# Optimization experiments

Hardware: AMD Instinct MI355X
Metric: run time of the kernel (lower is better)

## Reference

```python
import jax, jax.numpy as jnp
import numpy as np

HEADDIM = 128
CHUNK = 256


def _ssd_scan(x, dt, A, B, C, chunk):
    # x: (b,l,h,p)  dt: (b,l,h)  A: (h,)  B,C: (b,l,n)  (single group g=1 shared by all heads)
    b, l, h, p = x.shape
    n = B.shape[-1]
    nc = l // chunk
    dA = dt * A  # (b,l,h)
    xc = x.reshape(b, nc, chunk, h, p)
    dtc = dt.reshape(b, nc, chunk, h)
    dAc = dA.reshape(b, nc, chunk, h)
    Bc = B.reshape(b, nc, chunk, n)
    Cc = C.reshape(b, nc, chunk, n)
    cs = jnp.cumsum(dAc, axis=2)  # (b,nc,c,h) cumulative log-decay within chunk
    # intra-chunk quadratic part
    CB = jnp.einsum('bjin,bjkn->bjik', Cc, Bc)  # (b,nc,c,c)
    decay = jnp.exp(cs[:, :, :, None, :] - cs[:, :, None, :, :])  # (b,nc,i,k,h)
    mask = jnp.tril(jnp.ones((chunk, chunk), dtype=bool))
    decay = jnp.where(mask[None, None, :, :, None], decay, 0.0)
    y_intra = jnp.einsum('bjik,bjikh,bjkh,bjkhp->bjihp', CB, decay, dtc, xc)
    # per-chunk end states
    decay_states = jnp.exp(cs[:, :, -1:, :] - cs)  # (b,nc,c,h)
    states = jnp.einsum('bjkh,bjkh,bjkn,bjkhp->bjhnp', decay_states, dtc, Bc, xc)
    # recurrence across chunks: h_j = exp(sum dA_j) * h_{j-1} + states_j
    chunk_decay = jnp.exp(cs[:, :, -1, :])  # (b,nc,h)
    def step(carry, inp):
        s, d = inp
        new = carry * d[:, :, None, None] + s
        return new, carry  # emit state BEFORE this chunk
    init = jnp.zeros((b, h, n, p), x.dtype)
    _, prev = jax.lax.scan(step, init,
                           (states.transpose(1, 0, 2, 3, 4), chunk_decay.transpose(1, 0, 2)))
    prev = prev.transpose(1, 0, 2, 3, 4)  # (b,nc,h,n,p)
    y_inter = jnp.einsum('bjih,bjin,bjhnp->bjihp', jnp.exp(cs), Cc, prev)
    return (y_intra + y_inter).reshape(b, l, h, p)


def setup_inputs() -> dict:
    key = jax.random.key(0)
    k1, k2, k3, k4 = jax.random.split(key, 4)
    b, l, d_inner, nheads, d_state = 2, 4096, 2048, 16, 256
    x = jax.random.normal(k1, (b, l, d_inner), dtype=jnp.float32)
    BC = jax.random.normal(k2, (b, l, 2 * d_state), dtype=jnp.float32) * 0.1
    dt = jax.random.normal(k3, (b, l, 2 * nheads), dtype=jnp.float32) - 3.0
    A_log = jnp.zeros((nheads,), dtype=jnp.float32)
    D = jnp.ones((nheads,), dtype=jnp.float32)
    W_fcD = jax.random.normal(k4, (nheads, d_inner), dtype=jnp.float32) * 0.02
    return {"x": x, "BC": BC, "dt": dt, "A_log": A_log, "D": D, "W_fcD": W_fcD}


def reference(x, BC, dt, A_log, D, W_fcD):
    b, l, dim = x.shape
    h = A_log.shape[0]
    p = HEADDIM
    d_state = BC.shape[-1] // 2
    A = -jnp.exp(A_log)
    # bidirectional: concat forward stream with time-flipped backward stream along batch
    dt2 = jnp.concatenate((dt[:, :, :h], jnp.flip(dt[:, :, h:], axis=1)), axis=0)
    dt2 = jax.nn.softplus(dt2)
    x_og = x
    x2 = jnp.concatenate((x, jnp.flip(x, axis=1)), axis=0)
    BC2 = jnp.concatenate((BC, jnp.flip(BC, axis=1)), axis=0)
    B, C = BC2[..., :d_state], BC2[..., d_state:]
    y = _ssd_scan(x2.reshape(2 * b, l, h, p), dt2, A, B, C, CHUNK)
    y = y.reshape(2 * b, l, dim)
    y = jnp.roll(y, shift=1, axis=1).at[:, 0, :].set(0.0)
    y_fw, y_bw = y[:b], jnp.flip(y[b:], axis=1)
    gate = x_og @ W_fcD.T + D  # (b,l,h)
    y = y_fw + y_bw + x_og * jnp.repeat(gate, p, axis=-1)
    return y
```

## Files before the change

### kernel.cpp

```cpp
#include <hip/hip_runtime.h>
#include <stdint.h>

#define NB 2
#define SL 4096
#define NH 16
#define HD 128
#define DS 256
#define CK 256
#define NCH 16
#define NSQ 4
#define DI 2048

#define EPST 132

typedef unsigned short u16;
typedef unsigned int u32;
typedef __attribute__((ext_vector_type(8))) __bf16 bf16x8;
typedef __attribute__((ext_vector_type(4))) float f32x4;

__device__ __forceinline__ int tor(int dir, int t) { return dir ? (SL - 1 - t) : t; }

__device__ __forceinline__ u16 f2bf(float f) {
  u32 u = __float_as_uint(f);
  u = u + 0x7fffu + ((u >> 16) & 1u);
  return (u16)(u >> 16);
}
__device__ __forceinline__ float bf2f(u16 s) {
  return __uint_as_float(((u32)s) << 16);
}

struct Stg { uint4 a, b; };

__device__ __forceinline__ Stg ld_tile(const u16* __restrict__ src, int row, int q0, int k0) {
  const uint4* p = (const uint4*)(src + (size_t)row * 256 + k0 + (q0 << 3));
  Stg s; s.a = p[0]; s.b = p[1]; return s;
}
__device__ __forceinline__ void st_tile(u16* buf, int row, int q0, Stg s) {
  int sw = (row >> 1) & 3;
  *(uint4*)&buf[row * 32 + ((q0 ^ sw) << 3)] = s.a;
  *(uint4*)&buf[row * 32 + (((q0 + 1) ^ sw) << 3)] = s.b;
}

__device__ __forceinline__ bf16x8 frag(const u16* lds, int base_row, int m, int quad) {
  int row = base_row + m;
  return *(const bf16x8*)&lds[row * 32 + ((quad ^ ((row >> 1) & 3)) << 3)];
}

__device__ __forceinline__ void mfma16(const u16* As, const u16* Bs, int wi, int wp,
                                       int m, int quad, f32x4 acc[4][4]) {
  bf16x8 af[4], bv[4];
#pragma unroll
  for (int r = 0; r < 4; ++r) af[r] = frag(As, wi + (r << 4), m, quad);
#pragma unroll
  for (int c = 0; c < 4; ++c) bv[c] = frag(Bs, wp + (c << 4), m, quad);
#pragma unroll
  for (int r = 0; r < 4; ++r)
#pragma unroll
    for (int c = 0; c < 4; ++c)
      acc[r][c] = __builtin_amdgcn_mfma_f32_16x16x32_bf16(af[r], bv[c], acc[r][c], 0, 0, 0);
}

__global__ __launch_bounds__(256) void kprep(const float* __restrict__ dt,
                                             const float* __restrict__ A_log,
                                             float* __restrict__ csb,
                                             float* __restrict__ dtvb,
                                             float* __restrict__ cdecb) {
  int blk = blockIdx.x;
  int h = blk & 15, sj = blk >> 4;
  int s = sj >> 4, j = sj & 15;
  int b = s & 1, dir = s >> 1;
  int i = threadIdx.x;
  int to = tor(dir, j * CK + i);
  __shared__ float sbuf[CK];
  float a = -expf(A_log[h]);
  float raw = dt[((size_t)(b * SL + to)) * (2 * NH) + dir * NH + h];
  float sp = (raw > 20.f) ? raw : log1pf(expf(raw));
  sbuf[i] = sp * a;
  __syncthreads();
  for (int off = 1; off < CK; off <<= 1) {
    float v = (i >= off) ? sbuf[i - off] : 0.f;
    __syncthreads();
    sbuf[i] += v;
    __syncthreads();
  }
  float csv = sbuf[i];
  size_t base = ((size_t)sj * NH + h) * CK;
  csb[base + i] = csv;
  dtvb[base + i] = sp;
  if (i == CK - 1) cdecb[sj * NH + h] = expf(csv);
}

__global__ __launch_bounds__(256) void kcastT(const float* __restrict__ BC,
                                              u16* __restrict__ Bbf,
                                              u16* __restrict__ Cbf,
                                              u16* __restrict__ BbfT) {
  int blk = blockIdx.x;
  int kq = blk & 3, sj = blk >> 2;
  int s = sj >> 4, j = sj & 15;
  int b = s & 1, dir = s >> 1;
  __shared__ u16 T[64 * 264];
  int tid = threadIdx.x;
  int r = tid >> 2, part = (tid & 3) * 64;
  int t = j * CK + kq * 64 + r;
  int tsrc = tor(dir, t);
  const float* src = BC + ((size_t)(b * SL + tsrc)) * (2 * DS);
  size_t dstb = ((size_t)s * SL + t) * DS;
  u16 bb[64], cc[64];
#pragma unroll
  for (int q = 0; q < 16; ++q) {
    float4 v = ((const float4*)(src + part))[q];
    bb[q * 4 + 0] = f2bf(v.x); bb[q * 4 + 1] = f2bf(v.y);
    bb[q * 4 + 2] = f2bf(v.z); bb[q * 4 + 3] = f2bf(v.w);
    float4 c = ((const float4*)(src + DS + part))[q];
    cc[q * 4 + 0] = f2bf(c.x); cc[q * 4 + 1] = f2bf(c.y);
    cc[q * 4 + 2] = f2bf(c.z); cc[q * 4 + 3] = f2bf(c.w);
  }
#pragma unroll
  for (int q = 0; q < 8; ++q) {
    ((uint4*)(Bbf + dstb + part))[q] = *(const uint4*)&bb[q * 8];
    ((uint4*)(Cbf + dstb + part))[q] = *(const uint4*)&cc[q * 8];
    *(uint4*)&T[r * 264 + part + q * 8] = *(const uint4*)&bb[q * 8];
  }
  __syncthreads();
  int n = tid;
  u16 col[64];
#pragma unroll
  for (int kk = 0; kk < 64; ++kk) col[kk] = T[kk * 264 + n];
  uint4* ds_ = (uint4*)(BbfT + (size_t)sj * DS * CK + (size_t)n * CK + kq * 64);
#pragma unroll
  for (int q = 0; q < 8; ++q) {
    uint4 wv;
    wv.x = (u32)col[q * 8 + 0] | ((u32)col[q * 8 + 1] << 16);
    wv.y = (u32)col[q * 8 + 2] | ((u32)col[q * 8 + 3] << 16);
    wv.z = (u32)col[q * 8 + 4] | ((u32)col[q * 8 + 5] << 16);
    wv.w = (u32)col[q * 8 + 6] | ((u32)col[q * 8 + 7] << 16);
    ds_[q] = wv;
  }
}

__global__ __launch_bounds__(256) void kxsT(const float* __restrict__ xg,
                                            const float* __restrict__ csb,
                                            const float* __restrict__ dtvb,
                                            u16* __restrict__ xsT) {
  int inst = blockIdx.x;
  int h = inst & 15, sj = inst >> 4;
  int s = sj >> 4, j = sj & 15;
  int b = s & 1, dir = s >> 1;
  int tid = threadIdx.x;
  __shared__ u16 Ls[128 * 40];
  size_t cbase = ((size_t)sj * NH + h) * CK;
  u16* dst = xsT + (size_t)inst * (128 * 256);
  int kk = tid >> 3;
  int pg = (tid & 7) * 16;
  int p2 = tid >> 1, half = tid & 1;
  float4 v[4];
  {
    int t = tor(dir, j * CK + kk);
    const float* src = xg + ((size_t)(b * SL + t)) * DI + h * HD + pg;
    v[0] = ((const float4*)src)[0]; v[1] = ((const float4*)src)[1];
    v[2] = ((const float4*)src)[2]; v[3] = ((const float4*)src)[3];
  }
  for (int k0 = 0; k0 < CK; k0 += 32) {
    int kglob = k0 + kk;
    float sc_ = expf(-csb[cbase + kglob]) * dtvb[cbase + kglob];
    float vv[16] = {v[0].x, v[0].y, v[0].z, v[0].w, v[1].x, v[1].y, v[1].z, v[1].w,
                    v[2].x, v[2].y, v[2].z, v[2].w, v[3].x, v[3].y, v[3].z, v[3].w};
    __syncthreads();
#pragma unroll
    for (int q = 0; q < 16; ++q) Ls[(pg + q) * 40 + kk] = f2bf(vv[q] * sc_);
    if (k0 + 32 < CK) {
      int t = tor(dir, j * CK + k0 + 32 + kk);
      const float* src = xg + ((size_t)(b * SL + t)) * DI + h * HD + pg;
      v[0] = ((const float4*)src)[0]; v[1] = ((const float4*)src)[1];
      v[2] = ((const float4*)src)[2]; v[3] = ((const float4*)src)[3];
    }
    __syncthreads();
    uint4 w0 = *(const uint4*)&Ls[p2 * 40 + half * 16];
    uint4 w1 = *(const uint4*)&Ls[p2 * 40 + half * 16 + 8];
    *(uint4*)&dst[(size_t)p2 * 256 + k0 + half * 16] = w0;
    *(uint4*)&dst[(size_t)p2 * 256 + k0 + half * 16 + 8] = w1;
  }
}

__global__ __launch_bounds__(256) void kcb(const u16* __restrict__ Cbf,
                                           const u16* __restrict__ Bbf,
                                           u16* __restrict__ CBm) {
  int blk = blockIdx.x;
  int tri = blk % 3;
  int sj = blk / 3;
  int it0 = tri ? 128 : 0;
  int kt0 = (tri == 2) ? 128 : 0;
  int s = sj >> 4, j = sj & 15;
  __shared__ u16 smem[128 * EPST];
  int tid = threadIdx.x;
  int w = tid >> 6, lane = tid & 63;
  int wi = (w >> 1) << 6, wp = (w & 1) << 6;
  int m = lane & 15, quad = lane >> 4;
  int row = tid >> 1, q0 = (tid & 1) << 1;
  const u16* Ab = Cbf + ((size_t)s * SL + j * CK + it0) * DS;
  const u16* Bb = Bbf + ((size_t)s * SL + j * CK + kt0) * DS;
  f32x4 zini = {0.f, 0.f, 0.f, 0.f};
  f32x4 acc[4][4];
#pragma unroll
  for (int r = 0; r < 4; ++r)
#pragma unroll
    for (int c = 0; c < 4; ++c) acc[r][c] = zini;
  const int n = 8;
  Stg pa = ld_tile(Ab, row, q0, 0);
  Stg pb = ld_tile(Bb, row, q0, 0);
  st_tile(smem, row, q0, pa);
  st_tile(smem + 8192, row, q0, pb);
  Stg a1 = ld_tile(Ab, row, q0, 32);
  Stg b1 = ld_tile(Bb, row, q0, 32);
  Stg a2 = ld_tile(Ab, row, q0, 64);
  Stg b2 = ld_tile(Bb, row, q0, 64);
  for (int ks = 1; ks < n; ++ks) {
    __syncthreads();
    int cur = (ks & 1) << 12;
    st_tile(smem + cur, row, q0, a1);
    st_tile(smem + 8192 + cur, row, q0, b1);
    a1 = a2; b1 = b2;
    if (ks + 2 < n) {
      a2 = ld_tile(Ab, row, q0, (ks + 2) << 5);
      b2 = ld_tile(Bb, row, q0, (ks + 2) << 5);
    }
    int prv = ((ks - 1) & 1) << 12;
    mfma16(smem + prv, smem + 8192 + prv, wi, wp, m, quad, acc);
  }
  __syncthreads();
  {
    int prv = ((n - 1) & 1) << 12;
    mfma16(smem + prv, smem + 8192 + prv, wi, wp, m, quad, acc);
  }
  __syncthreads();
  int diag = (it0 == kt0);
#pragma unroll
  for (int r = 0; r < 4; ++r)
#pragma unroll
    for (int rg = 0; rg < 4; ++rg) {
      int irow = wi + (r << 4) + (quad << 2) + rg;
#pragma unroll
      for (int c = 0; c < 4; ++c) {
        int kcol = wp + (c << 4) + m;
        float v = acc[r][c][rg];
        if (diag && kcol > irow) v = 0.f;
        smem[irow * EPST + kcol] = f2bf(v);
      }
    }
  __syncthreads();
  {
    u16* dstb = CBm + ((size_t)sj * CK + it0) * CK + kt0;
    int rr = tid >> 1, off = (tid & 1) << 6;
    const uint4* srcv = (const uint4*)&smem[rr * EPST + off];
    uint4* dstv = (uint4*)(dstb + (size_t)rr * CK + off);
#pragma unroll
    for (int q = 0; q < 8; ++q) dstv[q] = srcv[q];
  }
}

__global__ __launch_bounds__(256) void kstates(const u16* __restrict__ xsT,
                                               const u16* __restrict__ BbfT,
                                               const float* __restrict__ cdecb,
                                               u16* __restrict__ prevT) {
  int blk = blockIdx.x;
  int ntile = blk & 1;
  int inst = blk >> 1;
  int h = inst & 15, sj = inst >> 4;
  int nt0 = ntile << 7;
  __shared__ u16 smem[128 * EPST];
  int tid = threadIdx.x;
  int w = tid >> 6, lane = tid & 63;
  int wi = (w >> 1) << 6, wp = (w & 1) << 6;
  int m = lane & 15, quad = lane >> 4;
  int row = tid >> 1, q0 = (tid & 1) << 1;
  const u16* Ab = xsT + (size_t)inst * (128 * 256);
  const u16* Bb = BbfT + ((size_t)sj * DS + nt0) * CK;
  f32x4 zini = {0.f, 0.f, 0.f, 0.f};
  f32x4 acc[4][4];
#pragma unroll
  for (int r = 0; r < 4; ++r)
#pragma unroll
    for (int c = 0; c < 4; ++c) acc[r][c] = zini;
  const int n = 8;
  Stg pa = ld_tile(Ab, row, q0, 0);
  Stg pb = ld_tile(Bb, row, q0, 0);
  st_tile(smem, row, q0, pa);
  st_tile(smem + 8192, row, q0, pb);
  Stg a1 = ld_tile(Ab, row, q0, 32);
  Stg b1 = ld_tile(Bb, row, q0, 32);
  Stg a2 = ld_tile(Ab, row, q0, 64);
  Stg b2 = ld_tile(Bb, row, q0, 64);
  for (int ks = 1; ks < n; ++ks) {
    __syncthreads();
    int cur = (ks & 1) << 12;
    st_tile(smem + cur, row, q0, a1);
    st_tile(smem + 8192 + cur, row, q0, b1);
    a1 = a2; b1 = b2;
    if (ks + 2 < n) {
      a2 = ld_tile(Ab, row, q0, (ks + 2) << 5);
      b2 = ld_tile(Bb, row, q0, (ks + 2) << 5);
    }
    int prv = ((ks - 1) & 1) << 12;
    mfma16(smem + prv, smem + 8192 + prv, wi, wp, m, quad, acc);
  }
  __syncthreads();
  {
    int prv = ((n - 1) & 1) << 12;
    mfma16(smem + prv, smem + 8192 + prv, wi, wp, m, quad, acc);
  }
  __syncthreads();
  float scale = cdecb[sj * NH + h];
#pragma unroll
  for (int r = 0; r < 4; ++r)
#pragma unroll
    for (int rg = 0; rg < 4; ++rg) {
      int prow = wi + (r << 4) + (quad << 2) + rg;
#pragma unroll
      for (int c = 0; c < 4; ++c) {
        int ncol = wp + (c << 4) + m;
        smem[prow * EPST + ncol] = f2bf(acc[r][c][rg] * scale);
      }
    }
  __syncthreads();
  {
    u16* dstb = prevT + (size_t)inst * (128 * 256) + nt0;
    int rr = tid >> 1, off = (tid & 1) << 6;
    const uint4* srcv = (const uint4*)&smem[rr * EPST + off];
    uint4* dstv = (uint4*)(dstb + (size_t)rr * 256 + off);
#pragma unroll
    for (int q = 0; q < 8; ++q) dstv[q] = srcv[q];
  }
}

__global__ __launch_bounds__(256) void kscan(u16* __restrict__ prevT,
                                             const float* __restrict__ cdecb) {
  int g = blockIdx.x * 256 + threadIdx.x;
  int n0 = (g & 31) * 8;
  int p = (g >> 5) & 127;
  int h = (g >> 12) & 15;
  int s = g >> 16;
  size_t base = ((size_t)(s * 256 + h) * 128 + p) * 256 + n0;
  const size_t stride = (size_t)NH * 128 * 256;
  float carry[8] = {0.f, 0.f, 0.f, 0.f, 0.f, 0.f, 0.f, 0.f};
  uint4 u = *(const uint4*)&prevT[base];
  for (int j = 0; j < NCH; ++j) {
    size_t idx = base + (size_t)j * stride;
    uint4 un;
    if (j + 1 < NCH) un = *(const uint4*)&prevT[idx + stride];
    u32 uu[4] = {u.x, u.y, u.z, u.w};
    float sv[8];
#pragma unroll
    for (int q = 0; q < 4; ++q) {
      sv[2 * q] = __uint_as_float(uu[q] << 16);
      sv[2 * q + 1] = __uint_as_float(uu[q] & 0xffff0000u);
    }
    uint4 wv;
    wv.x = (u32)f2bf(carry[0]) | ((u32)f2bf(carry[1]) << 16);
    wv.y = (u32)f2bf(carry[2]) | ((u32)f2bf(carry[3]) << 16);
    wv.z = (u32)f2bf(carry[4]) | ((u32)f2bf(carry[5]) << 16);
    wv.w = (u32)f2bf(carry[6]) | ((u32)f2bf(carry[7]) << 16);
    *(uint4*)&prevT[idx] = wv;
    float d = cdecb[(s * NCH + j) * NH + h];
#pragma unroll
    for (int q = 0; q < 8; ++q) carry[q] = carry[q] * d + sv[q];
    u = un;
  }
}

__global__ __launch_bounds__(256) void ky(const u16* __restrict__ CBm,
                                          const u16* __restrict__ Cbf,
                                          const u16* __restrict__ xsT,
                                          const u16* __restrict__ prevT,
                                          const float* __restrict__ csb,
                                          u16* __restrict__ ytmpb) {
  int blk = blockIdx.x;
  int itile = blk & 1;
  int inst = blk >> 1;
  int h = inst & 15, sj = inst >> 4;
  int s = sj >> 4, j = sj & 15;
  int it0 = itile << 7;
  __shared__ u16 smem[128 * EPST];
  int tid = threadIdx.x;
  int w = tid >> 6, lane = tid & 63;
  int wi = (w >> 1) << 6, wp = (w & 1) << 6;
  int m = lane & 15, quad = lane >> 4;
  int row = tid >> 1, q0 = (tid & 1) << 1;

  const u16* Ai = CBm + ((size_t)sj * CK + it0) * CK;
  const u16* Ae = Cbf + ((size_t)s * SL + j * CK + it0) * DS;
  const u16* Bi = xsT + (size_t)inst * (128 * 256);
  const u16* Be = prevT + (size_t)inst * (128 * 256);

  int nIntra = itile ? 8 : 4;
  int n = nIntra + 8;

  f32x4 zini = {0.f, 0.f, 0.f, 0.f};
  f32x4 acc[4][4];
#pragma unroll
  for (int r = 0; r < 4; ++r)
#pragma unroll
    for (int c = 0; c < 4; ++c) acc[r][c] = zini;

#define KY_SRC(ks, Ap, Bp, kk)                                  \
  {                                                             \
    int intra_ = (ks) < nIntra;                                 \
    kk = (intra_ ? (ks) : (ks) - nIntra) << 5;                  \
    Ap = intra_ ? Ai : Ae;                                      \
    Bp = intra_ ? Bi : Be;                                      \
  }

  const u16 *Ap, *Bp; int kk;
  KY_SRC(0, Ap, Bp, kk);
  Stg pa = ld_tile(Ap, row, q0, kk);
  Stg pb = ld_tile(Bp, row, q0, kk);
  st_tile(smem, row, q0, pa);
  st_tile(smem + 8192, row, q0, pb);
  KY_SRC(1, Ap, Bp, kk);
  Stg a1 = ld_tile(Ap, row, q0, kk);
  Stg b1 = ld_tile(Bp, row, q0, kk);
  KY_SRC(2, Ap, Bp, kk);
  Stg a2 = ld_tile(Ap, row, q0, kk);
  Stg b2 = ld_tile(Bp, row, q0, kk);
  for (int ks = 1; ks < n; ++ks) {
    __syncthreads();
    int cur = (ks & 1) << 12;
    st_tile(smem + cur, row, q0, a1);
    st_tile(smem + 8192 + cur, row, q0, b1);
    a1 = a2; b1 = b2;
    if (ks + 2 < n) {
      KY_SRC(ks + 2, Ap, Bp, kk);
      a2 = ld_tile(Ap, row, q0, kk);
      b2 = ld_tile(Bp, row, q0, kk);
    }
    int prv = ((ks - 1) & 1) << 12;
    mfma16(smem + prv, smem + 8192 + prv, wi, wp, m, quad, acc);
  }
  __syncthreads();
  {
    int prv = ((n - 1) & 1) << 12;
    mfma16(smem + prv, smem + 8192 + prv, wi, wp, m, quad, acc);
  }
  __syncthreads();
#undef KY_SRC

  const float* csrow = csb + ((size_t)sj * NH + h) * CK + it0;
#pragma unroll
  for (int r = 0; r < 4; ++r)
#pragma unroll
    for (int rg = 0; rg < 4; ++rg) {
      int irow = wi + (r << 4) + (quad << 2) + rg;
      float esc = expf(csrow[irow]);
#pragma unroll
      for (int c = 0; c < 4; ++c) {
        int pcol = wp + (c << 4) + m;
        smem[irow * EPST + pcol] = f2bf(acc[r][c][rg] * esc);
      }
    }
  __syncthreads();
  {
    u16* yb = ytmpb + ((size_t)s * SL + j * CK + it0) * DI + h * HD;
    int rr = tid >> 1, off = (tid & 1) << 6;
    const uint4* srcv = (const uint4*)&smem[rr * EPST + off];
    uint4* dstv = (uint4*)(yb + (size_t)rr * DI + off);
#pragma unroll
    for (int q = 0; q < 8; ++q) dstv[q] = srcv[q];
  }
}

__global__ __launch_bounds__(256) void kwt(const float* __restrict__ Wg,
                                           float* __restrict__ WT) {
  int g = blockIdx.x * 256 + threadIdx.x;
  int d = g >> 4, h = g & 15;
  WT[g] = Wg[(size_t)h * DI + d];
}

__global__ __launch_bounds__(256) void kgate(const float* __restrict__ xg,
                                             const float* __restrict__ WT,
                                             const float* __restrict__ Dg,
                                             float* __restrict__ gate) {
  int wave = (blockIdx.x * 256 + threadIdx.x) >> 6;
  int lane = threadIdx.x & 63;
  int gg = lane >> 4, h = lane & 15;
  int row0 = wave * 8;
  const float* xb = xg + (size_t)row0 * DI;
  float acc[8] = {0.f, 0.f, 0.f, 0.f, 0.f, 0.f, 0.f, 0.f};
  for (int q = 0; q < 128; ++q) {
    int d = gg * 4 + 16 * q;
    float w0 = WT[(d + 0) * 16 + h];
    float w1 = WT[(d + 1) * 16 + h];
    float w2 = WT[(d + 2) * 16 + h];
    float w3 = WT[(d + 3) * 16 + h];
#pragma unroll
    for (int r = 0; r < 8; ++r) {
      float4 xv = *(const float4*)&xb[(size_t)r * DI + d];
      acc[r] += xv.x * w0 + xv.y * w1 + xv.z * w2 + xv.w * w3;
    }
  }
#pragma unroll
  for (int r = 0; r < 8; ++r) {
    acc[r] += __shfl_down(acc[r], 32);
    acc[r] += __shfl_down(acc[r], 16);
  }
  if (lane < 16) {
    float dv = Dg[h];
#pragma unroll
    for (int r = 0; r < 8; ++r) gate[(size_t)(row0 + r) * NH + h] = acc[r] + dv;
  }
}

__device__ __forceinline__ void unpk8(uint4 u, float* o) {
  o[0] = __uint_as_float(u.x << 16); o[1] = __uint_as_float(u.x & 0xffff0000u);
  o[2] = __uint_as_float(u.y << 16); o[3] = __uint_as_float(u.y & 0xffff0000u);
  o[4] = __uint_as_float(u.z << 16); o[5] = __uint_as_float(u.z & 0xffff0000u);
  o[6] = __uint_as_float(u.w << 16); o[7] = __uint_as_float(u.w & 0xffff0000u);
}

__global__ __launch_bounds__(256) void kcombine(const float* __restrict__ xg,
                                                const float* __restrict__ gate,
                                                const u16* __restrict__ ytmpb,
                                                float* __restrict__ out) {
  int bid = blockIdx.x;
  int b = bid >> 12;
  int t = bid & (SL - 1);
  int tid = threadIdx.x;
  int d0 = tid * 8;
  float g = gate[(size_t)(b * SL + t) * NH + (tid >> 4)];
  float fy[8] = {0.f, 0.f, 0.f, 0.f, 0.f, 0.f, 0.f, 0.f};
  float by[8] = {0.f, 0.f, 0.f, 0.f, 0.f, 0.f, 0.f, 0.f};
  if (t > 0) {
    uint4 u = *(const uint4*)(ytmpb + ((size_t)(b * SL + (t - 1))) * DI + d0);
    unpk8(u, fy);
  }
  if (t < SL - 1) {
    uint4 u = *(const uint4*)(ytmpb + ((size_t)((2 + b) * SL + (SL - 2 - t))) * DI + d0);
    unpk8(u, by);
  }
  const float* xr = xg + ((size_t)(b * SL + t)) * DI + d0;
  float4 x0 = ((const float4*)xr)[0];
  float4 x1 = ((const float4*)xr)[1];
  float xa[8] = {x0.x, x0.y, x0.z, x0.w, x1.x, x1.y, x1.z, x1.w};
  float* op = out + ((size_t)(b * SL + t)) * DI + d0;
  float4 o0, o1;
  o0.x = fy[0] + by[0] + xa[0] * g; o0.y = fy[1] + by[1] + xa[1] * g;
  o0.z = fy[2] + by[2] + xa[2] * g; o0.w = fy[3] + by[3] + xa[3] * g;
  o1.x = fy[4] + by[4] + xa[4] * g; o1.y = fy[5] + by[5] + xa[5] * g;
  o1.z = fy[6] + by[6] + xa[6] * g; o1.w = fy[7] + by[7] + xa[7] * g;
  ((float4*)op)[0] = o0;
  ((float4*)op)[1] = o1;
}

extern "C" void kernel_launch(void* const* d_in, const int* in_sizes, int n_in,
                              void* d_out, int out_size, void* d_ws, size_t ws_size,
                              hipStream_t stream) {
  (void)in_sizes; (void)n_in; (void)out_size; (void)ws_size;
  const float* x     = (const float*)d_in[0];
  const float* BC    = (const float*)d_in[1];
  const float* dt    = (const float*)d_in[2];
  const float* A_log = (const float*)d_in[3];
  const float* Dg    = (const float*)d_in[4];
  const float* W     = (const float*)d_in[5];
  float* out = (float*)d_out;

  char* p = (char*)d_ws;
  float* cs   = (float*)p;  p += (size_t)NSQ * NCH * NH * CK * 4;
  float* dtv  = (float*)p;  p += (size_t)NSQ * NCH * NH * CK * 4;
  float* cdec = (float*)p;  p += (size_t)NSQ * NCH * NH * 4;
  float* WT   = (float*)p;  p += (size_t)DI * NH * 4;
  float* gateb= (float*)p;  p += (size_t)NB * SL * NH * 4;
  u16* Bbf    = (u16*)p;    p += (size_t)NSQ * SL * DS * 2;
  u16* Cbf    = (u16*)p;    p += (size_t)NSQ * SL * DS * 2;
  u16* BbfT   = (u16*)p;    p += (size_t)NSQ * NCH * DS * CK * 2;
  u16* CBm    = (u16*)p;    p += (size_t)NSQ * NCH * CK * CK * 2;
  u16* xsT    = (u16*)p;    p += (size_t)NSQ * NCH * NH * HD * CK * 2;
  u16* prevT  = (u16*)p;    p += (size_t)NSQ * NCH * NH * HD * DS * 2;
  u16* ytmpb  = (u16*)p;    p += (size_t)NSQ * SL * DI * 2;

  hipLaunchKernelGGL(kprep,   dim3(NSQ * NCH * NH),      dim3(CK),  0, stream, dt, A_log, cs, dtv, cdec);
  hipLaunchKernelGGL(kcastT,  dim3(NSQ * NCH * 4),       dim3(256), 0, stream, BC, Bbf, Cbf, BbfT);
  hipLaunchKernelGGL(kcb,     dim3(NSQ * NCH * 3),       dim3(256), 0, stream, Cbf, Bbf, CBm);
  hipLaunchKernelGGL(kxsT,    dim3(NSQ * NCH * NH),      dim3(256), 0, stream, x, cs, dtv, xsT);
  hipLaunchKernelGGL(kwt,     dim3(DI * NH / 256),       dim3(256), 0, stream, W, WT);
  hipLaunchKernelGGL(kgate,   dim3(NB * SL / 32),        dim3(256), 0, stream, x, WT, Dg, gateb);
  hipLaunchKernelGGL(kstates, dim3(NSQ * NCH * NH * 2),  dim3(256), 0, stream, xsT, BbfT, cdec, prevT);
  hipLaunchKernelGGL(kscan,   dim3(NSQ * NH * HD * DS / (256 * 8)), dim3(256), 0, stream, prevT, cdec);
  hipLaunchKernelGGL(ky,      dim3(NSQ * NCH * NH * 2),  dim3(256), 0, stream, CBm, Cbf, xsT, prevT, cs, ytmpb);
  hipLaunchKernelGGL(kcombine,dim3(NB * SL),             dim3(256), 0, stream, x, gateb, ytmpb, out);
}
```

Measured before the change: 421.6 us.

## Fuse x scaling into chunk-state GEMM, widen ky K-tiles, drop W transpose

Merges the kxsT and kstates kernels so each block scales and casts its x chunk, keeps the whole scaled chunk in LDS, and runs both state N-tiles from it. Global re-reads of xsT and one launch go away, but the block now holds a large LDS footprint (about 80 KB), which lowers occupancy. The ky kernel moves to 64-wide K tiles with a new swizzle and single-stage prefetch, which halves the barrier count. kcb's prefetch depth shrinks to one stage, and kgate reads W directly as float4 so the kwt transpose kernel is dropped.

```diff
diff --git a/kernel.cpp b/kernel.cpp
--- a/kernel.cpp
+++ b/kernel.cpp
@@ -40,12 +40,10 @@
   *(uint4*)&buf[row * 32 + ((q0 ^ sw) << 3)] = s.a;
   *(uint4*)&buf[row * 32 + (((q0 + 1) ^ sw) << 3)] = s.b;
 }
-
 __device__ __forceinline__ bf16x8 frag(const u16* lds, int base_row, int m, int quad) {
   int row = base_row + m;
   return *(const bf16x8*)&lds[row * 32 + ((quad ^ ((row >> 1) & 3)) << 3)];
 }
-
 __device__ __forceinline__ void mfma16(const u16* As, const u16* Bs, int wi, int wp,
                                        int m, int quad, f32x4 acc[4][4]) {
   bf16x8 af[4], bv[4];
@@ -58,6 +56,42 @@
 #pragma unroll
     for (int c = 0; c < 4; ++c)
       acc[r][c] = __builtin_amdgcn_mfma_f32_16x16x32_bf16(af[r], bv[c], acc[r][c], 0, 0, 0);
+}
+
+struct Stg64 { uint4 v[4]; };
+
+__device__ __forceinline__ Stg64 ld_t64(const u16* __restrict__ src, int row, int half, int k0) {
+  const uint4* p = (const uint4*)(src + (size_t)row * 256 + k0 + half * 32);
+  Stg64 s;
+#pragma unroll
+  for (int c = 0; c < 4; ++c) s.v[c] = p[c];
+  return s;
+}
+__device__ __forceinline__ void st_t64(u16* buf, int row, int half, Stg64 s) {
+  int sw = row & 7;
+#pragma unroll
+  for (int c = 0; c < 4; ++c)
+    *(uint4*)&buf[row * 64 + (((half * 4 + c) ^ sw) << 3)] = s.v[c];
+}
+__device__ __forceinline__ bf16x8 frag64(const u16* lds, int base_row, int m, int quad, int cb) {
+  int row = base_row + m;
+  return *(const bf16x8*)&lds[row * 64 + (((cb + quad) ^ (row & 7)) << 3)];
+}
+__device__ __forceinline__ void mfma64(const u16* As, const u16* Bs, int wi, int wp,
+                                       int m, int quad, f32x4 acc[4][4]) {
+#pragma unroll
+  for (int cb = 0; cb < 8; cb += 4) {
+    bf16x8 af[4], bv[4];
+#pragma unroll
+    for (int r = 0; r < 4; ++r) af[r] = frag64(As, wi + (r << 4), m, quad, cb);
+#pragma unroll
+    for (int c = 0; c < 4; ++c) bv[c] = frag64(Bs, wp + (c << 4), m, quad, cb);
+#pragma unroll
+    for (int r = 0; r < 4; ++r)
+#pragma unroll
+      for (int c = 0; c < 4; ++c)
+        acc[r][c] = __builtin_amdgcn_mfma_f32_16x16x32_bf16(af[r], bv[c], acc[r][c], 0, 0, 0);
+  }
 }
 
 __global__ __launch_bounds__(256) void kprep(const float* __restrict__ dt,
@@ -135,50 +169,6 @@
     wv.z = (u32)col[q * 8 + 4] | ((u32)col[q * 8 + 5] << 16);
     wv.w = (u32)col[q * 8 + 6] | ((u32)col[q * 8 + 7] << 16);
     ds_[q] = wv;
-  }
-}
-
-__global__ __launch_bounds__(256) void kxsT(const float* __restrict__ xg,
-                                            const float* __restrict__ csb,
-                                            const float* __restrict__ dtvb,
-                                            u16* __restrict__ xsT) {
-  int inst = blockIdx.x;
-  int h = inst & 15, sj = inst >> 4;
-  int s = sj >> 4, j = sj & 15;
-  int b = s & 1, dir = s >> 1;
-  int tid = threadIdx.x;
-  __shared__ u16 Ls[128 * 40];
-  size_t cbase = ((size_t)sj * NH + h) * CK;
-  u16* dst = xsT + (size_t)inst * (128 * 256);
-  int kk = tid >> 3;
-  int pg = (tid & 7) * 16;
-  int p2 = tid >> 1, half = tid & 1;
-  float4 v[4];
-  {
-    int t = tor(dir, j * CK + kk);
-    const float* src = xg + ((size_t)(b * SL + t)) * DI + h * HD + pg;
-    v[0] = ((const float4*)src)[0]; v[1] = ((const float4*)src)[1];
-    v[2] = ((const float4*)src)[2]; v[3] = ((const float4*)src)[3];
-  }
-  for (int k0 = 0; k0 < CK; k0 += 32) {
-    int kglob = k0 + kk;
-    float sc_ = expf(-csb[cbase + kglob]) * dtvb[cbase + kglob];
-    float vv[16] = {v[0].x, v[0].y, v[0].z, v[0].w, v[1].x, v[1].y, v[1].z, v[1].w,
-                    v[2].x, v[2].y, v[2].z, v[2].w, v[3].x, v[3].y, v[3].z, v[3].w};
-    __syncthreads();
-#pragma unroll
-    for (int q = 0; q < 16; ++q) Ls[(pg + q) * 40 + kk] = f2bf(vv[q] * sc_);
-    if (k0 + 32 < CK) {
-      int t = tor(dir, j * CK + k0 + 32 + kk);
-      const float* src = xg + ((size_t)(b * SL + t)) * DI + h * HD + pg;
-      v[0] = ((const float4*)src)[0]; v[1] = ((const float4*)src)[1];
-      v[2] = ((const float4*)src)[2]; v[3] = ((const float4*)src)[3];
-    }
-    __syncthreads();
-    uint4 w0 = *(const uint4*)&Ls[p2 * 40 + half * 16];
-    uint4 w1 = *(const uint4*)&Ls[p2 * 40 + half * 16 + 8];
-    *(uint4*)&dst[(size_t)p2 * 256 + k0 + half * 16] = w0;
-    *(uint4*)&dst[(size_t)p2 * 256 + k0 + half * 16 + 8] = w1;
   }
 }
 
@@ -210,19 +200,16 @@
   Stg pb = ld_tile(Bb, row, q0, 0);
   st_tile(smem, row, q0, pa);
   st_tile(smem + 8192, row, q0, pb);
-  Stg a1 = ld_tile(Ab, row, q0, 32);
-  Stg b1 = ld_tile(Bb, row, q0, 32);
-  Stg a2 = ld_tile(Ab, row, q0, 64);
-  Stg b2 = ld_tile(Bb, row, q0, 64);
+  pa = ld_tile(Ab, row, q0, 32);
+  pb = ld_tile(Bb, row, q0, 32);
   for (int ks = 1; ks < n; ++ks) {
     __syncthreads();
     int cur = (ks & 1) << 12;
-    st_tile(smem + cur, row, q0, a1);
-    st_tile(smem + 8192 + cur, row, q0, b1);
-    a1 = a2; b1 = b2;
-    if (ks + 2 < n) {
-      a2 = ld_tile(Ab, row, q0, (ks + 2) << 5);
-      b2 = ld_tile(Bb, row, q0, (ks + 2) << 5);
+    st_tile(smem + cur, row, q0, pa);
+    st_tile(smem + 8192 + cur, row, q0, pb);
+    if (ks + 1 < n) {
+      pa = ld_tile(Ab, row, q0, (ks + 1) << 5);
+      pb = ld_tile(Bb, row, q0, (ks + 1) << 5);
     }
     int prv = ((ks - 1) & 1) << 12;
     mfma16(smem + prv, smem + 8192 + prv, wi, wp, m, quad, acc);
@@ -258,77 +245,94 @@
   }
 }
 
-__global__ __launch_bounds__(256) void kstates(const u16* __restrict__ xsT,
-                                               const u16* __restrict__ BbfT,
-                                               const float* __restrict__ cdecb,
-                                               u16* __restrict__ prevT) {
-  int blk = blockIdx.x;
-  int ntile = blk & 1;
-  int inst = blk >> 1;
+__global__ __launch_bounds__(256) void kxstates(const float* __restrict__ xg,
+                                                const float* __restrict__ csb,
+                                                const float* __restrict__ dtvb,
+                                                const float* __restrict__ cdecb,
+                                                const u16* __restrict__ BbfT,
+                                                u16* __restrict__ xsT,
+                                                u16* __restrict__ prevT) {
+  int inst = blockIdx.x;
   int h = inst & 15, sj = inst >> 4;
-  int nt0 = ntile << 7;
-  __shared__ u16 smem[128 * EPST];
+  int s = sj >> 4, j = sj & 15;
+  int b = s & 1, dir = s >> 1;
+  __shared__ u16 xs[8 * 4096];
+  __shared__ u16 un[8192];
   int tid = threadIdx.x;
+
+  size_t cbase = ((size_t)sj * NH + h) * CK;
+  u16* gdst = xsT + (size_t)inst * (128 * 256);
+  int kk = tid >> 3;
+  int pg = (tid & 7) * 16;
+  int p2 = tid >> 1, half = tid & 1;
+  float4 v[4];
+  {
+    int t = tor(dir, j * CK + kk);
+    const float* src = xg + ((size_t)(b * SL + t)) * DI + h * HD + pg;
+    v[0] = ((const float4*)src)[0]; v[1] = ((const float4*)src)[1];
+    v[2] = ((const float4*)src)[2]; v[3] = ((const float4*)src)[3];
+  }
+  for (int k0 = 0; k0 < CK; k0 += 32) {
+    int kglob = k0 + kk;
+    float sc_ = expf(-csb[cbase + kglob]) * dtvb[cbase + kglob];
+    float vv[16] = {v[0].x, v[0].y, v[0].z, v[0].w, v[1].x, v[1].y, v[1].z, v[1].w,
+                    v[2].x, v[2].y, v[2].z, v[2].w, v[3].x, v[3].y, v[3].z, v[3].w};
+    __syncthreads();
+#pragma unroll
+    for (int q = 0; q < 16; ++q) un[(pg + q) * 40 + kk] = f2bf(vv[q] * sc_);
+    if (k0 + 32 < CK) {
+      int t = tor(dir, j * CK + k0 + 32 + kk);
+      const float* src = xg + ((size_t)(b * SL + t)) * DI + h * HD + pg;
+      v[0] = ((const float4*)src)[0]; v[1] = ((const float4*)src)[1];
+      v[2] = ((const float4*)src)[2]; v[3] = ((const float4*)src)[3];
+    }
+    __syncthreads();
+    uint4 w0 = *(const uint4*)&un[p2 * 40 + half * 16];
+    uint4 w1 = *(const uint4*)&un[p2 * 40 + half * 16 + 8];
+    *(uint4*)&gdst[(size_t)p2 * 256 + k0 + half * 16] = w0;
+    *(uint4*)&gdst[(size_t)p2 * 256 + k0 + half * 16 + 8] = w1;
+    Stg sg; sg.a = w0; sg.b = w1;
+    st_tile(xs + (k0 >> 5) * 4096, p2, half * 2, sg);
+  }
+  __syncthreads();
+
   int w = tid >> 6, lane = tid & 63;
   int wi = (w >> 1) << 6, wp = (w & 1) << 6;
   int m = lane & 15, quad = lane >> 4;
   int row = tid >> 1, q0 = (tid & 1) << 1;
-  const u16* Ab = xsT + (size_t)inst * (128 * 256);
-  const u16* Bb = BbfT + ((size_t)sj * DS + nt0) * CK;
-  f32x4 zini = {0.f, 0.f, 0.f, 0.f};
-  f32x4 acc[4][4];
-#pragma unroll
-  for (int r = 0; r < 4; ++r)
-#pragma unroll
-    for (int c = 0; c < 4; ++c) acc[r][c] = zini;
-  const int n = 8;
-  Stg pa = ld_tile(Ab, row, q0, 0);
-  Stg pb = ld_tile(Bb, row, q0, 0);
-  st_tile(smem, row, q0, pa);
-  st_tile(smem + 8192, row, q0, pb);
-  Stg a1 = ld_tile(Ab, row, q0, 32);
-  Stg b1 = ld_tile(Bb, row, q0, 32);
-  Stg a2 = ld_tile(Ab, row, q0, 64);
-  Stg b2 = ld_tile(Bb, row, q0, 64);
-  for (int ks = 1; ks < n; ++ks) {
-    __syncthreads();
-    int cur = (ks & 1) << 12;
-    st_tile(smem + cur, row, q0, a1);
-    st_tile(smem + 8192 + cur, row, q0, b1);
-    a1 = a2; b1 = b2;
-    if (ks + 2 < n) {
-      a2 = ld_tile(Ab, row, q0, (ks + 2) << 5);
-      b2 = ld_tile(Bb, row, q0, (ks + 2) << 5);
-    }
-    int prv = ((ks - 1) & 1) << 12;
-    mfma16(smem + prv, smem + 8192 + prv, wi, wp, m, quad, acc);
-  }
-  __syncthreads();
-  {
-    int prv = ((n - 1) & 1) << 12;
-    mfma16(smem + prv, smem + 8192 + prv, wi, wp, m, quad, acc);
-  }
-  __syncthreads();
   float scale = cdecb[sj * NH + h];
-#pragma unroll
-  for (int r = 0; r < 4; ++r)
-#pragma unroll
-    for (int rg = 0; rg < 4; ++rg) {
-      int prow = wi + (r << 4) + (quad << 2) + rg;
-#pragma unroll
-      for (int c = 0; c < 4; ++c) {
-        int ncol = wp + (c << 4) + m;
-        smem[prow * EPST + ncol] = f2bf(acc[r][c][rg] * scale);
+  for (int ntile = 0; ntile < 2; ++ntile) {
+    const u16* Bb = BbfT + ((size_t)sj * DS + (ntile << 7)) * CK;
+    f32x4 zini = {0.f, 0.f, 0.f, 0.f};
+    f32x4 acc[4][4];
+#pragma unroll
+    for (int r = 0; r < 4; ++r)
+#pragma unroll
+      for (int c = 0; c < 4; ++c) acc[r][c] = zini;
+    Stg pb = ld_tile(Bb, row, q0, 0);
+    st_tile(un, row, q0, pb);
+    pb = ld_tile(Bb, row, q0, 32);
+    for (int ks = 1; ks < 8; ++ks) {
+      __syncthreads();
+      st_tile(un + ((ks & 1) << 12), row, q0, pb);
+      if (ks + 1 < 8) pb = ld_tile(Bb, row, q0, (ks + 1) << 5);
+      mfma16(xs + ((ks - 1) << 12), un + (((ks - 1) & 1) << 12), wi, wp, m, quad, acc);
+    }
+    __syncthreads();
+    mfma16(xs + (7 << 12), un + ((7 & 1) << 12), wi, wp, m, quad, acc);
+    u16* dstb = prevT + (size_t)inst * (128 * 256) + (ntile << 7);
+#pragma unroll
+    for (int r = 0; r < 4; ++r)
+#pragma unroll
+      for (int rg = 0; rg < 4; ++rg) {
+        int prow = wi + (r << 4) + (quad << 2) + rg;
+#pragma unroll
+        for (int c = 0; c < 4; ++c) {
+          int ncol = wp + (c << 4) + m;
+          dstb[(size_t)prow * 256 + ncol] = f2bf(acc[r][c][rg] * scale);
+        }
       }
-    }
-  __syncthreads();
-  {
-    u16* dstb = prevT + (size_t)inst * (128 * 256) + nt0;
-    int rr = tid >> 1, off = (tid & 1) << 6;
-    const uint4* srcv = (const uint4*)&smem[rr * EPST + off];
-    uint4* dstv = (uint4*)(dstb + (size_t)rr * 256 + off);
-#pragma unroll
-    for (int q = 0; q < 8; ++q) dstv[q] = srcv[q];
+    __syncthreads();
   }
 }
 
@@ -379,20 +383,20 @@
   int h = inst & 15, sj = inst >> 4;
   int s = sj >> 4, j = sj & 15;
   int it0 = itile << 7;
-  __shared__ u16 smem[128 * EPST];
+  __shared__ u16 smem[32768];
   int tid = threadIdx.x;
   int w = tid >> 6, lane = tid & 63;
   int wi = (w >> 1) << 6, wp = (w & 1) << 6;
   int m = lane & 15, quad = lane >> 4;
-  int row = tid >> 1, q0 = (tid & 1) << 1;
+  int row = tid >> 1, half = tid & 1;
 
   const u16* Ai = CBm + ((size_t)sj * CK + it0) * CK;
   const u16* Ae = Cbf + ((size_t)s * SL + j * CK + it0) * DS;
   const u16* Bi = xsT + (size_t)inst * (128 * 256);
   const u16* Be = prevT + (size_t)inst * (128 * 256);
 
-  int nIntra = itile ? 8 : 4;
-  int n = nIntra + 8;
+  int nI = itile ? 4 : 2;
+  int n = nI + 4;
 
   f32x4 zini = {0.f, 0.f, 0.f, 0.f};
   f32x4 acc[4][4];
@@ -401,44 +405,40 @@
 #pragma unroll
     for (int c = 0; c < 4; ++c) acc[r][c] = zini;
 
-#define KY_SRC(ks, Ap, Bp, kk)                                  \
+#define KY_SRC(ks)                                              \
   {                                                             \
-    int intra_ = (ks) < nIntra;                                 \
-    kk = (intra_ ? (ks) : (ks) - nIntra) << 5;                  \
+    int intra_ = (ks) < nI;                                     \
+    kk = (intra_ ? (ks) : (ks) - nI) << 6;                      \
     Ap = intra_ ? Ai : Ae;                                      \
     Bp = intra_ ? Bi : Be;                                      \
   }
 
   const u16 *Ap, *Bp; int kk;
-  KY_SRC(0, Ap, Bp, kk);
-  Stg pa = ld_tile(Ap, row, q0, kk);
-  Stg pb = ld_tile(Bp, row, q0, kk);
-  st_tile(smem, row, q0, pa);
-  st_tile(smem + 8192, row, q0, pb);
-  KY_SRC(1, Ap, Bp, kk);
-  Stg a1 = ld_tile(Ap, row, q0, kk);
-  Stg b1 = ld_tile(Bp, row, q0, kk);
-  KY_SRC(2, Ap, Bp, kk);
-  Stg a2 = ld_tile(Ap, row, q0, kk);
-  Stg b2 = ld_tile(Bp, row, q0, kk);
+  KY_SRC(0);
+  Stg64 a1 = ld_t64(Ap, row, half, kk);
+  Stg64 b1 = ld_t64(Bp, row, half, kk);
+  st_t64(smem, row, half, a1);
+  st_t64(smem + 16384, row, half, b1);
+  KY_SRC(1);
+  a1 = ld_t64(Ap, row, half, kk);
+  b1 = ld_t64(Bp, row, half, kk);
   for (int ks = 1; ks < n; ++ks) {
     __syncthreads();
-    int cur = (ks & 1) << 12;
-    st_tile(smem + cur, row, q0, a1);
-    st_tile(smem + 8192 + cur, row, q0, b1);
-    a1 = a2; b1 = b2;
-    if (ks + 2 < n) {
-      KY_SRC(ks + 2, Ap, Bp, kk);
-      a2 = ld_tile(Ap, row, q0, kk);
-      b2 = ld_tile(Bp, row, q0, kk);
-    }
-    int prv = ((ks - 1) & 1) << 12;
-    mfma16(smem + prv, smem + 8192 + prv, wi, wp, m, quad, acc);
+    int cur = (ks & 1) << 13;
+    st_t64(smem + cur, row, half, a1);
+    st_t64(smem + 16384 + cur, row, half, b1);
+    if (ks + 1 < n) {
+      KY_SRC(ks + 1);
+      a1 = ld_t64(Ap, row, half, kk);
+      b1 = ld_t64(Bp, row, half, kk);
+    }
+    int prv = ((ks - 1) & 1) << 13;
+    mfma64(smem + prv, smem + 16384 + prv, wi, wp, m, quad, acc);
   }
   __syncthreads();
   {
-    int prv = ((n - 1) & 1) << 12;
-    mfma16(smem + prv, smem + 8192 + prv, wi, wp, m, quad, acc);
+    int prv = ((n - 1) & 1) << 13;
+    mfma64(smem + prv, smem + 16384 + prv, wi, wp, m, quad, acc);
   }
   __syncthreads();
 #undef KY_SRC
@@ -467,15 +467,8 @@
   }
 }
 
-__global__ __launch_bounds__(256) void kwt(const float* __restrict__ Wg,
-                                           float* __restrict__ WT) {
-  int g = blockIdx.x * 256 + threadIdx.x;
-  int d = g >> 4, h = g & 15;
-  WT[g] = Wg[(size_t)h * DI + d];
-}
-
 __global__ __launch_bounds__(256) void kgate(const float* __restrict__ xg,
-                                             const float* __restrict__ WT,
+                                             const float* __restrict__ Wg,
                                              const float* __restrict__ Dg,
                                              float* __restrict__ gate) {
   int wave = (blockIdx.x * 256 + threadIdx.x) >> 6;
@@ -486,14 +479,11 @@
   float acc[8] = {0.f, 0.f, 0.f, 0.f, 0.f, 0.f, 0.f, 0.f};
   for (int q = 0; q < 128; ++q) {
     int d = gg * 4 + 16 * q;
-    float w0 = WT[(d + 0) * 16 + h];
-    float w1 = WT[(d + 1) * 16 + h];
-    float w2 = WT[(d + 2) * 16 + h];
-    float w3 = WT[(d + 3) * 16 + h];
+    float4 wv = *(const float4*)&Wg[(size_t)h * DI + d];
 #pragma unroll
     for (int r = 0; r < 8; ++r) {
       float4 xv = *(const float4*)&xb[(size_t)r * DI + d];
-      acc[r] += xv.x * w0 + xv.y * w1 + xv.z * w2 + xv.w * w3;
+      acc[r] += xv.x * wv.x + xv.y * wv.y + xv.z * wv.z + xv.w * wv.w;
     }
   }
 #pragma unroll
@@ -565,7 +555,6 @@
   float* cs   = (float*)p;  p += (size_t)NSQ * NCH * NH * CK * 4;
   float* dtv  = (float*)p;  p += (size_t)NSQ * NCH * NH * CK * 4;
   float* cdec = (float*)p;  p += (size_t)NSQ * NCH * NH * 4;
-  float* WT   = (float*)p;  p += (size_t)DI * NH * 4;
   float* gateb= (float*)p;  p += (size_t)NB * SL * NH * 4;
   u16* Bbf    = (u16*)p;    p += (size_t)NSQ * SL * DS * 2;
   u16* Cbf    = (u16*)p;    p += (size_t)NSQ * SL * DS * 2;
@@ -575,14 +564,12 @@
   u16* prevT  = (u16*)p;    p += (size_t)NSQ * NCH * NH * HD * DS * 2;
   u16* ytmpb  = (u16*)p;    p += (size_t)NSQ * SL * DI * 2;
 
-  hipLaunchKernelGGL(kprep,   dim3(NSQ * NCH * NH),      dim3(CK),  0, stream, dt, A_log, cs, dtv, cdec);
-  hipLaunchKernelGGL(kcastT,  dim3(NSQ * NCH * 4),       dim3(256), 0, stream, BC, Bbf, Cbf, BbfT);
-  hipLaunchKernelGGL(kcb,     dim3(NSQ * NCH * 3),       dim3(256), 0, stream, Cbf, Bbf, CBm);
-  hipLaunchKernelGGL(kxsT,    dim3(NSQ * NCH * NH),      dim3(256), 0, stream, x, cs, dtv, xsT);
-  hipLaunchKernelGGL(kwt,     dim3(DI * NH / 256),       dim3(256), 0, stream, W, WT);
-  hipLaunchKernelGGL(kgate,   dim3(NB * SL / 32),        dim3(256), 0, stream, x, WT, Dg, gateb);
-  hipLaunchKernelGGL(kstates, dim3(NSQ * NCH * NH * 2),  dim3(256), 0, stream, xsT, BbfT, cdec, prevT);
-  hipLaunchKernelGGL(kscan,   dim3(NSQ * NH * HD * DS / (256 * 8)), dim3(256), 0, stream, prevT, cdec);
-  hipLaunchKernelGGL(ky,      dim3(NSQ * NCH * NH * 2),  dim3(256), 0, stream, CBm, Cbf, xsT, prevT, cs, ytmpb);
-  hipLaunchKernelGGL(kcombine,dim3(NB * SL),             dim3(256), 0, stream, x, gateb, ytmpb, out);
-}
+  hipLaunchKernelGGL(kprep,    dim3(NSQ * NCH * NH),     dim3(CK),  0, stream, dt, A_log, cs, dtv, cdec);
+  hipLaunchKernelGGL(kcastT,   dim3(NSQ * NCH * 4),      dim3(256), 0, stream, BC, Bbf, Cbf, BbfT);
+  hipLaunchKernelGGL(kcb,      dim3(NSQ * NCH * 3),      dim3(256), 0, stream, Cbf, Bbf, CBm);
+  hipLaunchKernelGGL(kxstates, dim3(NSQ * NCH * NH),     dim3(256), 0, stream, x, cs, dtv, cdec, BbfT, xsT, prevT);
+  hipLaunchKernelGGL(kscan,    dim3(NSQ * NH * HD * DS / (256 * 8)), dim3(256), 0, stream, prevT, cdec);
+  hipLaunchKernelGGL(ky,       dim3(NSQ * NCH * NH * 2), dim3(256), 0, stream, CBm, Cbf, xsT, prevT, cs, ytmpb);
+  hipLaunchKernelGGL(kgate,    dim3(NB * SL / 32),       dim3(256), 0, stream, x, W, Dg, gateb);
+  hipLaunchKernelGGL(kcombine, dim3(NB * SL),            dim3(256), 0, stream, x, gateb, ytmpb, out);
+}
```

Result: slower. 443.5 us (+5.2%).
